# Performance work log

Hardware: AMD Instinct MI355X
Metric: run time of the kernel (lower is better)

The kernel has to match this reference:

```python
import jax, jax.numpy as jnp
import numpy as np
from jax import lax

ASPACE = 500
HEAD = 2
TEMP = 0.8
GEPS = 1e-20
LOG2PI = float(np.log(2.0 * np.pi))


def gru_cell(x, h, Wih, Whh, bih, bhh):
    # torch GRUCell math
    gi = x @ Wih.T + bih
    gh = h @ Whh.T + bhh
    i_r, i_z, i_n = jnp.split(gi, 3, axis=-1)
    h_r, h_z, h_n = jnp.split(gh, 3, axis=-1)
    r = jax.nn.sigmoid(i_r + h_r)
    z = jax.nn.sigmoid(i_z + h_z)
    n = jnp.tanh(i_n + r * h_n)
    return (1.0 - z) * n + z * h


def setup_inputs() -> dict:
    key = jax.random.key(0)
    ks = jax.random.split(key, 16)
    B, T, D, E = 128, 128, 300, 1024
    s = 0.05
    nrm = lambda k, shp: s * jax.random.normal(k, shp, dtype=jnp.float32)
    return {
        "x": jax.random.normal(ks[0], (B, T, D), dtype=jnp.float32),
        "lengths": jnp.full((B,), T, dtype=jnp.int32),  # full-length sequences
        "train": 1,
        # rl_rnn = GRUCell(300, 300)
        "Wih_cell": nrm(ks[1], (3 * D, D)),
        "Whh_cell": nrm(ks[2], (3 * D, D)),
        "bih_cell": nrm(ks[3], (3 * D,)),
        "bhh_cell": nrm(ks[4], (3 * D,)),
        # linear_rl_image_mus: 600 -> 1000
        "Wmu": nrm(ks[5], (ASPACE * HEAD, 2 * D)),
        "bmu": nrm(ks[6], (ASPACE * HEAD,)),
        # linear_logvars: 600 -> 2
        "Wlv": nrm(ks[7], (HEAD, 2 * D)),
        "blv": nrm(ks[8], (HEAD,)),
        # rnn = GRU(300, 1024, 1 layer)
        "Wih_rnn": nrm(ks[9], (3 * E, D)),
        "Whh_rnn": nrm(ks[10], (3 * E, E)),
        "bih_rnn": nrm(ks[11], (3 * E,)),
        "bhh_rnn": nrm(ks[12], (3 * E,)),
        # BatchNorm1d(1024)
        "bn_gamma": jnp.ones((E,), dtype=jnp.float32),
        "bn_beta": jnp.zeros((E,), dtype=jnp.float32),
    }


def _gumbel(key, shape):
    u = jax.random.uniform(key, shape, dtype=jnp.float32)
    return -jnp.log(-jnp.log(u + GEPS) + GEPS)


def reference(x, lengths, train, Wih_cell, Whh_cell, bih_cell, bhh_cell,
              Wmu, bmu, Wlv, blv, Wih_rnn, Whh_rnn, bih_rnn, bhh_rnn,
              bn_gamma, bn_beta):
    # train path only (train==1): stochastic gumbel-softmax + Normal sampling
    B, T, D = x.shape
    E = bn_gamma.shape[0]
    x = lax.stop_gradient(x)  # torch: x = x.detach()

    nk = jax.random.split(jax.random.key(42), 4)
    g_soft = _gumbel(nk[0], (T, B * HEAD, ASPACE))   # gumbel for softmax perturbation
    g_cat = _gumbel(nk[1], (T, B * HEAD, ASPACE))    # gumbel-max trick == multinomial
    eps1 = jax.random.normal(nk[2], (T, B, HEAD), dtype=jnp.float32)  # dist.sample()
    eps2 = jax.random.normal(nk[3], (T, B, HEAD), dtype=jnp.float32)  # second dist.sample() for log_prob

    arange_a = jnp.arange(ASPACE, dtype=jnp.float32)

    def step(hx, inputs):
        img, g, gc, e1, e2 = inputs  # img: [B,300]
        hx = gru_cell(img, hx, Wih_cell, Whh_cell, bih_cell, bhh_cell)
        cat = jax.nn.relu(jnp.concatenate([img, hx], axis=1))  # [B,600]
        mu = cat @ Wmu.T + bmu                                  # [B,1000]
        lv = jax.nn.softplus(cat @ Wlv.T + blv)                 # [B,2]
        logits = mu.reshape(B * HEAD, ASPACE)
        y = jax.nn.softmax((logits + g) / TEMP, axis=-1)
        ind = jnp.argmax(jnp.log(y) + gc, axis=-1)              # multinomial(y, 1)
        prob = jnp.take_along_axis(y, ind[:, None], axis=1)[:, 0]
        one_hot = jax.nn.one_hot(ind, ASPACE, dtype=y.dtype)
        y_hard = lax.stop_gradient(one_hot - y) + y             # straight-through
        action = (arange_a * y_hard).sum(-1).reshape(B, HEAD) / ASPACE  # [B,2]
        std = jnp.exp(0.5 * lv)                                 # [B,2]
        s1 = action + std * e1                                  # img_att sample
        s2 = action + std * e2                                  # sample used in log_prob
        logp = -0.5 * ((s2 - action) / std) ** 2 - jnp.log(std) - 0.5 * LOG2PI
        att = 20.0 * jax.nn.sigmoid(s1)                         # [B,2]
        text = (img.reshape(B, HEAD, D // HEAD) * att[:, :, None]).reshape(B, D)
        return hx, (action, jnp.log(prob).reshape(B, HEAD), logp, text)

    hx0 = jnp.zeros((B, D), dtype=x.dtype)
    xs = (x.transpose(1, 0, 2), g_soft, g_cat, eps1, eps2)
    _, (act, slog, logp, texts) = lax.scan(step, hx0, xs)
    # torch stacking/reshapes
    sampled_log_img_all = slog.transpose(1, 0, 2).reshape(B, HEAD, T)  # stack dim1 then view(B,H,T)
    action_imgs_all = act.transpose(1, 2, 0)                           # [B,2,T]
    log_all = logp.transpose(1, 2, 0)                                  # [B,2,T]

    # second-stage GRU over reconstructed sequence [T,B,300]
    def gru_step(h, xt):
        h = gru_cell(xt, h, Wih_rnn, Whh_rnn, bih_rnn, bhh_rnn)
        return h, h

    _, outs = lax.scan(gru_step, jnp.zeros((B, E), dtype=x.dtype), texts)  # [T,B,E]
    outs = outs.transpose(1, 0, 2)                                         # [B,T,E]
    last = outs[jnp.arange(B), lengths - 1]                                # gather last valid step

    # BatchNorm1d (training mode: batch stats, biased variance)
    mean = last.mean(axis=0)
    var = ((last - mean) ** 2).mean(axis=0)
    feature_end = bn_gamma * (last - mean) / jnp.sqrt(var + 1e-5) + bn_beta
    return (feature_end, sampled_log_img_all, action_imgs_all, log_all)
```

## Files before the change

### kernel.cpp

```cpp
#include <hip/hip_runtime.h>
#include <stdint.h>

#define TT 128
#define BB 128
#define DD 300
#define EE 1024
#define GG 900
#define NMU 1008
#define ASP 500
#define KP 608

#define OUT_SLOG 131072
#define OUT_ACT  163840
#define OUT_LOGP 196608

typedef unsigned int u32x4 __attribute__((ext_vector_type(4)));

__host__ __device__ static inline uint32_t rotl32(uint32_t x, int r){
  return (x << r) | (x >> (32 - r));
}

__host__ __device__ static inline void tf2x32(uint32_t k0, uint32_t k1,
                                              uint32_t x0, uint32_t x1,
                                              uint32_t* o0, uint32_t* o1){
  uint32_t ks2 = k0 ^ k1 ^ 0x1BD11BDAu;
#define TFR(r) { x0 += x1; x1 = rotl32(x1, r); x1 ^= x0; }
  x0 += k0; x1 += k1;
  TFR(13) TFR(15) TFR(26) TFR(6)
  x0 += k1; x1 += ks2 + 1u;
  TFR(17) TFR(29) TFR(16) TFR(24)
  x0 += ks2; x1 += k0 + 2u;
  TFR(13) TFR(15) TFR(26) TFR(6)
  x0 += k0; x1 += k1 + 3u;
  TFR(17) TFR(29) TFR(16) TFR(24)
  x0 += k1; x1 += ks2 + 4u;
  TFR(13) TFR(15) TFR(26) TFR(6)
  x0 += ks2; x1 += k0 + 5u;
#undef TFR
  *o0 = x0; *o1 = x1;
}

__device__ static inline uint32_t rng32(uint32_t k0, uint32_t k1, uint32_t idx){
  uint32_t a, b;
  tf2x32(k0, k1, 0u, idx, &a, &b);
  return a ^ b;
}

__device__ static inline float u01(uint32_t bits){
  return __uint_as_float((bits >> 9) | 0x3f800000u) - 1.0f;
}

__device__ static inline float jgumbel(uint32_t k0, uint32_t k1, uint32_t idx){
  float u = u01(rng32(k0, k1, idx));
  float l1 = logf(u + 1e-20f);
  return -logf(-l1 + 1e-20f);
}

__device__ static inline float erfinv32(float x){
  float w = -log1pf(-x * x);
  float p;
  if (w < 5.0f){
    w = w - 2.5f;
    p = 2.81022636e-08f;
    p = 3.43273939e-07f  + p * w;
    p = -3.5233877e-06f  + p * w;
    p = -4.39150654e-06f + p * w;
    p = 0.00021858087f   + p * w;
    p = -0.00125372503f  + p * w;
    p = -0.00417768164f  + p * w;
    p = 0.246640727f     + p * w;
    p = 1.50140941f      + p * w;
  } else {
    w = sqrtf(w) - 3.0f;
    p = -0.000200214257f;
    p = 0.000100950558f  + p * w;
    p = 0.00134934322f   + p * w;
    p = -0.00367342844f  + p * w;
    p = 0.00573950773f   + p * w;
    p = -0.0076224613f   + p * w;
    p = 0.00943887047f   + p * w;
    p = 1.00167406f      + p * w;
    p = 2.83297682f      + p * w;
  }
  return p * x;
}

__device__ static inline float jnormal(uint32_t k0, uint32_t k1, uint32_t idx){
  float u = u01(rng32(k0, k1, idx));
  const float lo = -0.99999994f;
  float v = u * 2.0f + lo;
  v = fmaxf(lo, v);
  return 1.41421356237f * erfinv32(v);
}

__device__ static inline float jsigmoid(float x){
  return 1.0f / (1.0f + expf(-x));
}

__device__ static inline unsigned short f2bf(float f){
  uint32_t u = __float_as_uint(f);
  uint32_t r = (u + 0x7fffu + ((u >> 16) & 1u)) >> 16;
  return (unsigned short)r;
}
__device__ static inline float bf2f(unsigned short h){
  return __uint_as_float((uint32_t)h << 16);
}

__device__ static inline u32x4 load_b128_llc(const void* p){
  u32x4 r;
  asm volatile("global_load_dwordx4 %0, %1, off sc0 sc1"
               : "=v"(r) : "v"(p) : "memory");
  return r;
}
__device__ static inline void store_b128_llc(void* p, u32x4 v){
  asm volatile("global_store_dwordx4 %0, %1, off sc0 sc1"
               :: "v"(p), "v"(v) : "memory");
}
__device__ static inline unsigned poll_u32_llc(const void* p){
  unsigned r;
  asm volatile("global_load_dword %0, %1, off sc0 sc1\n\ts_waitcnt vmcnt(0)"
               : "=v"(r) : "v"(p) : "memory");
  return r;
}
__device__ static inline void store_u32_llc(void* p, unsigned v){
  asm volatile("global_store_dword %0, %1, off sc0 sc1"
               :: "v"(p), "v"(v) : "memory");
}

#define WAITV(N) do{ asm volatile("s_waitcnt vmcnt(" #N ")" ::: "memory"); \
                     __builtin_amdgcn_sched_barrier(0); }while(0)

#define FMA4(ACC, S, B) { ACC.x += (S)*(B).x; ACC.y += (S)*(B).y; \
                          ACC.z += (S)*(B).z; ACC.w += (S)*(B).w; }

__global__ __launch_bounds__(256) void k_gemm_gi(
    const float* __restrict__ X, const float* __restrict__ W,
    const float* __restrict__ bias, float* __restrict__ C)
{
  __shared__ float As[16][132];
  __shared__ float Bs[16][68];
  const int tid = threadIdx.x;
  const int rbase = blockIdx.y * 128;
  const int cbase = blockIdx.x * 64;
  const int tx = tid & 15, ty = tid >> 4;
  const int sr = tid >> 2, sq = tid & 3;
  const int wj = cbase + sr;

  float4 acc[8];
#pragma unroll
  for (int i = 0; i < 8; ++i) acc[i] = (float4){0,0,0,0};

  for (int k0 = 0; k0 < 304; k0 += 16){
    const int k = k0 + sq * 4;
#pragma unroll
    for (int i = 0; i < 2; ++i){
      const int row = sr + i * 64;
      const int rg = rbase + row;
      float4 va = {0,0,0,0};
      if (k < DD) va = *(const float4*)(X + ((long)(rg & 127) * TT + (rg >> 7)) * DD + k);
      As[sq*4+0][row] = va.x; As[sq*4+1][row] = va.y;
      As[sq*4+2][row] = va.z; As[sq*4+3][row] = va.w;
    }
    {
      float4 vb = {0,0,0,0};
      if (k < DD && wj < GG) vb = *(const float4*)(W + (long)wj * DD + k);
      Bs[sq*4+0][sr] = vb.x; Bs[sq*4+1][sr] = vb.y;
      Bs[sq*4+2][sr] = vb.z; Bs[sq*4+3][sr] = vb.w;
    }
    __syncthreads();
#pragma unroll
    for (int kk = 0; kk < 16; ++kk){
      const float4 b  = *(const float4*)&Bs[kk][tx * 4];
      const float4 a0 = *(const float4*)&As[kk][ty * 8];
      const float4 a1 = *(const float4*)&As[kk][ty * 8 + 4];
      FMA4(acc[0], a0.x, b); FMA4(acc[1], a0.y, b);
      FMA4(acc[2], a0.z, b); FMA4(acc[3], a0.w, b);
      FMA4(acc[4], a1.x, b); FMA4(acc[5], a1.y, b);
      FMA4(acc[6], a1.z, b); FMA4(acc[7], a1.w, b);
    }
    __syncthreads();
  }
  const int ci = cbase + tx * 4;
  float bv[4];
#pragma unroll
  for (int j = 0; j < 4; ++j) bv[j] = (ci + j < GG) ? bias[ci + j] : 0.0f;
#pragma unroll
  for (int i = 0; i < 8; ++i){
    const int r = rbase + ty * 8 + i;
    float vals[4] = {acc[i].x + bv[0], acc[i].y + bv[1],
                     acc[i].z + bv[2], acc[i].w + bv[3]};
    float* crow = C + (long)r * GG;
    if (ci + 3 < GG){
      float4 st = {vals[0], vals[1], vals[2], vals[3]};
      *(float4*)(crow + ci) = st;
    } else {
#pragma unroll
      for (int j = 0; j < 4; ++j) if (ci + j < GG) crow[ci + j] = vals[j];
    }
  }
}

__global__ __launch_bounds__(256) void k_cvt_Amu(
    const float* __restrict__ X, const float* __restrict__ HX,
    unsigned short* __restrict__ Ah, unsigned short* __restrict__ Al)
{
  const long i = (long)blockIdx.x * 256 + threadIdx.x;
  const int r = (int)(i / 152), g = (int)(i - (long)r * 152);
  const int k = g * 4;
  const int b = r & 127, t = r >> 7;
  float4 v = {0,0,0,0};
  if (k < 300)      v = *(const float4*)(X + ((long)b * TT + t) * DD + k);
  else if (k < 600) v = *(const float4*)(HX + (long)r * DD + (k - 300));
  float vv[4] = {fmaxf(v.x,0.f), fmaxf(v.y,0.f), fmaxf(v.z,0.f), fmaxf(v.w,0.f)};
  unsigned short hi[4], lo[4];
#pragma unroll
  for (int j = 0; j < 4; ++j){
    hi[j] = f2bf(vv[j]);
    lo[j] = f2bf(vv[j] - bf2f(hi[j]));
  }
  const long off = (long)r * KP + k;
  *(uint2*)(Ah + off) = *(const uint2*)hi;
  *(uint2*)(Al + off) = *(const uint2*)lo;
}

__global__ __launch_bounds__(256) void k_cvt_Wmu(
    const float* __restrict__ Wmu, const float* __restrict__ Wlv,
    unsigned short* __restrict__ Wh, unsigned short* __restrict__ Wl)
{
  const long i = (long)blockIdx.x * 256 + threadIdx.x;
  const int r = (int)(i / 152), g = (int)(i - (long)r * 152);
  const int k = g * 4;
  float4 v = {0,0,0,0};
  if (k < 600){
    if (r < 1000)      v = *(const float4*)(Wmu + (long)r * 600 + k);
    else if (r < 1002) v = *(const float4*)(Wlv + (long)(r - 1000) * 600 + k);
  }
  float vv[4] = {v.x, v.y, v.z, v.w};
  unsigned short hi[4], lo[4];
#pragma unroll
  for (int j = 0; j < 4; ++j){
    hi[j] = f2bf(vv[j]);
    lo[j] = f2bf(vv[j] - bf2f(hi[j]));
  }
  const long off = (long)r * KP + k;
  *(uint2*)(Wh + off) = *(const uint2*)hi;
  *(uint2*)(Wl + off) = *(const uint2*)lo;
}

__global__ __launch_bounds__(256) void k_bias_mu(
    const float* __restrict__ bmu, const float* __restrict__ blv,
    float* __restrict__ bias)
{
  const int i = blockIdx.x * 256 + threadIdx.x;
  if (i < 1024){
    float v = 0.0f;
    if (i < 1000) v = bmu[i];
    else if (i < 1002) v = blv[i - 1000];
    bias[i] = v;
  }
}

__global__ __launch_bounds__(256) void k_gemm_mf(
    const unsigned short* __restrict__ Ah, const unsigned short* __restrict__ Al,
    const unsigned short* __restrict__ Bh, const unsigned short* __restrict__ Bl,
    const float* __restrict__ bias, float* __restrict__ C)
{
  __shared__ __align__(16) unsigned short sAh[128][40], sAl[128][40];
  __shared__ __align__(16) unsigned short sBh[64][40], sBl[64][40];
  const int tid = threadIdx.x;
  const int cbase = blockIdx.x * 64, rbase = blockIdx.y * 128;
  const int wave = tid >> 6, wm = wave >> 1, wn = wave & 1;
  const int lane = tid & 63, lo = lane & 15, hi4 = lane >> 4;

  using frag = __attribute__((ext_vector_type(8))) short;
  using f32x4 = __attribute__((ext_vector_type(4))) float;
  f32x4 acc[4][2];
#pragma unroll
  for (int a = 0; a < 4; ++a)
#pragma unroll
    for (int c = 0; c < 2; ++c) acc[a][c] = (f32x4){0.f,0.f,0.f,0.f};

  const int arow = tid >> 1, akh = (tid & 1) * 16;
  const int brow = tid >> 2, bkh = (tid & 3) * 8;

  for (int kb = 0; kb < 19; ++kb){
    const int k0 = kb * 32;
    __syncthreads();
    {
      const unsigned short* pa = Ah + (long)(rbase + arow) * KP + k0 + akh;
      *(uint4*)&sAh[arow][akh]     = *(const uint4*)pa;
      *(uint4*)&sAh[arow][akh + 8] = *(const uint4*)(pa + 8);
      const unsigned short* pl = Al + (long)(rbase + arow) * KP + k0 + akh;
      *(uint4*)&sAl[arow][akh]     = *(const uint4*)pl;
      *(uint4*)&sAl[arow][akh + 8] = *(const uint4*)(pl + 8);
      *(uint4*)&sBh[brow][bkh] = *(const uint4*)(Bh + (long)(cbase + brow) * KP + k0 + bkh);
      *(uint4*)&sBl[brow][bkh] = *(const uint4*)(Bl + (long)(cbase + brow) * KP + k0 + bkh);
    }
    __syncthreads();
    frag bh0 = *(const frag*)&sBh[wn*32 + lo][hi4*8];
    frag bh1 = *(const frag*)&sBh[wn*32 + 16 + lo][hi4*8];
    frag bl0 = *(const frag*)&sBl[wn*32 + lo][hi4*8];
    frag bl1 = *(const frag*)&sBl[wn*32 + 16 + lo][hi4*8];
#pragma unroll
    for (int fr = 0; fr < 4; ++fr){
      frag ah = *(const frag*)&sAh[wm*64 + fr*16 + lo][hi4*8];
      frag al = *(const frag*)&sAl[wm*64 + fr*16 + lo][hi4*8];
      acc[fr][0] = __builtin_amdgcn_mfma_f32_16x16x32_bf16(ah, bh0, acc[fr][0], 0, 0, 0);
      acc[fr][0] = __builtin_amdgcn_mfma_f32_16x16x32_bf16(al, bh0, acc[fr][0], 0, 0, 0);
      acc[fr][0] = __builtin_amdgcn_mfma_f32_16x16x32_bf16(ah, bl0, acc[fr][0], 0, 0, 0);
      acc[fr][0] = __builtin_amdgcn_mfma_f32_16x16x32_bf16(al, bl0, acc[fr][0], 0, 0, 0);
      acc[fr][1] = __builtin_amdgcn_mfma_f32_16x16x32_bf16(ah, bh1, acc[fr][1], 0, 0, 0);
      acc[fr][1] = __builtin_amdgcn_mfma_f32_16x16x32_bf16(al, bh1, acc[fr][1], 0, 0, 0);
      acc[fr][1] = __builtin_amdgcn_mfma_f32_16x16x32_bf16(ah, bl1, acc[fr][1], 0, 0, 0);
      acc[fr][1] = __builtin_amdgcn_mfma_f32_16x16x32_bf16(al, bl1, acc[fr][1], 0, 0, 0);
    }
  }
#pragma unroll
  for (int fr = 0; fr < 4; ++fr)
#pragma unroll
    for (int fc = 0; fc < 2; ++fc){
      const int col = cbase + wn*32 + fc*16 + lo;
      if (col < NMU){
        const float bv = bias[col];
        const int r0 = rbase + wm*64 + fr*16 + hi4*4;
#pragma unroll
        for (int j = 0; j < 4; ++j)
          C[(long)(r0 + j) * NMU + col] = acc[fr][fc][j] + bv;
      }
    }
}

__global__ __launch_bounds__(256) void k_pack_w3(
    const float* __restrict__ W, unsigned short* __restrict__ Wb3)
{
  const int g = blockIdx.x * 256 + threadIdx.x;
  if (g >= 245760) return;
  const int k4 = g % 80;
  const int r2 = g / 80;
  const int row = r2 % 64;
  const int r3 = r2 / 64;
  const int s = r3 % 3;
  const int js = r3 / 3;
  const int wid = (js < 15) ? 19 : 15;
  const int jj0 = js * 19;
  unsigned short o4[4];
#pragma unroll
  for (int e = 0; e < 4; ++e){
    const int k = k4 * 4 + e;
    float v = 0.0f;
    if (row < 3 * wid && k < 300){
      const int gate = row / wid, col = row - gate * wid;
      v = W[(long)(gate * 300 + jj0 + col) * 300 + k];
    }
    const unsigned short w1 = f2bf(v);
    const float r1 = v - bf2f(w1);
    const unsigned short w2 = f2bf(r1);
    const float r2f = r1 - bf2f(w2);
    const unsigned short w3 = f2bf(r2f);
    o4[e] = (s == 0) ? w1 : ((s == 1) ? w2 : w3);
  }
  *(uint2*)(Wb3 + ((long)(js * 3 + s) * 64 + row) * 320 + k4 * 4) = *(const uint2*)o4;
}

#define S1PAD 304

__global__ __launch_bounds__(256, 1) void k_stage1(
    const unsigned short* __restrict__ Wb3, const float* __restrict__ bhh,
    const float* __restrict__ gi_all, float* __restrict__ hx_all,
    float* __restrict__ hex, unsigned int* __restrict__ flagsA)
{
  __shared__ __align__(16) float hs[8][S1PAD];
  __shared__ __align__(16) unsigned short hb[3][8][320];
  __shared__ float ghs[512];
  const int tid = threadIdx.x;
  const int bid = blockIdx.x;
  const int bq = bid >> 4, js = bid & 15;
  const int b0 = bq * 8;
  const int wid = (js < 15) ? 19 : 15;
  const int jj0 = js * 19;
  const int NC = 3 * wid;

  const int wave = tid >> 6, lane = tid & 63;
  const int lo = lane & 15, hi = lane >> 4;

  using frag = __attribute__((ext_vector_type(8))) short;
  using f32x4v = __attribute__((ext_vector_type(4))) float;

  frag wfr[3][10];
  {
    const int row = wave * 16 + lo;
#pragma unroll
    for (int s = 0; s < 3; ++s)
#pragma unroll
      for (int kf = 0; kf < 10; ++kf)
        wfr[s][kf] = *(const frag*)(Wb3 + ((long)(js * 3 + s) * 64 + row) * 320
                                         + kf * 32 + hi * 8);
  }

  const bool gact = tid < 8 * wid;
  const int grow = gact ? (tid / wid) : 0;
  const int gcol = gact ? (tid - grow * wid) : 0;
  const int gjj = jj0 + gcol;
  float bhr = 0.f, bhz = 0.f, bhn = 0.f;
  if (gact){ bhr = bhh[gjj]; bhz = bhh[DD + gjj]; bhn = bhh[2*DD + gjj]; }

  for (int i = tid; i < 8 * S1PAD; i += 256) ((float*)hs)[i] = 0.f;
  for (int i = tid; i < 3840; i += 256) ((unsigned int*)hb)[i] = 0u;
  __syncthreads();

  unsigned int* myflag = flagsA + bid * 16;

  for (int t = 0; t < TT; ++t){
    float gir = 0.f, giz = 0.f, gin = 0.f;
    if (gact){
      const float* gp = gi_all + ((long)t * BB + b0 + grow) * GG;
      gir = gp[gjj]; giz = gp[DD + gjj]; gin = gp[2*DD + gjj];
    }

    f32x4v a0 = {0,0,0,0}, a1 = {0,0,0,0}, a2 = {0,0,0,0};
#pragma unroll
    for (int kf = 0; kf < 10; ++kf){
      frag h1 = *(const frag*)&hb[0][lo & 7][kf * 32 + hi * 8];
      frag h2 = *(const frag*)&hb[1][lo & 7][kf * 32 + hi * 8];
      frag h3 = *(const frag*)&hb[2][lo & 7][kf * 32 + hi * 8];
      a0 = __builtin_amdgcn_mfma_f32_16x16x32_bf16(h1, wfr[0][kf], a0, 0, 0, 0);
      a1 = __builtin_amdgcn_mfma_f32_16x16x32_bf16(h1, wfr[1][kf], a1, 0, 0, 0);
      a2 = __builtin_amdgcn_mfma_f32_16x16x32_bf16(h1, wfr[2][kf], a2, 0, 0, 0);
      a0 = __builtin_amdgcn_mfma_f32_16x16x32_bf16(h2, wfr[0][kf], a0, 0, 0, 0);
      a1 = __builtin_amdgcn_mfma_f32_16x16x32_bf16(h2, wfr[1][kf], a1, 0, 0, 0);
      a2 = __builtin_amdgcn_mfma_f32_16x16x32_bf16(h2, wfr[2][kf], a2, 0, 0, 0);
      a0 = __builtin_amdgcn_mfma_f32_16x16x32_bf16(h3, wfr[0][kf], a0, 0, 0, 0);
      a1 = __builtin_amdgcn_mfma_f32_16x16x32_bf16(h3, wfr[1][kf], a1, 0, 0, 0);
      a2 = __builtin_amdgcn_mfma_f32_16x16x32_bf16(h3, wfr[2][kf], a2, 0, 0, 0);
    }
    {
      const int nc = wave * 16 + lo;
      if (hi < 2 && nc < NC){
#pragma unroll
        for (int j = 0; j < 4; ++j)
          ghs[nc * 8 + hi * 4 + j] = (a0[j] + a1[j]) + a2[j];
      }
    }
    __syncthreads();

    const int par = t & 1;
    if (gact){
      const float r = jsigmoid(gir + ghs[(0 * wid + gcol) * 8 + grow] + bhr);
      const float z = jsigmoid(giz + ghs[(1 * wid + gcol) * 8 + grow] + bhz);
      const float n = tanhf(gin + r * (ghs[(2 * wid + gcol) * 8 + grow] + bhn));
      const float hn = (1.0f - z) * n + z * hs[grow][gjj];
      hx_all[((long)t * BB + b0 + grow) * DD + gjj] = hn;
      if (t < TT - 1)
        store_u32_llc(hex + ((long)par * BB + b0 + grow) * S1PAD + gjj,
                      __float_as_uint(hn));
    }

    if (t < TT - 1){
      asm volatile("s_waitcnt vmcnt(0)" ::: "memory");
      __syncthreads();
      if (tid == 0) store_u32_llc(myflag, (unsigned)(t + 1));
      if (tid < 16){
        const unsigned int* fp = flagsA + (bq * 16 + tid) * 16;
        unsigned v = poll_u32_llc(fp);
        while (v < (unsigned)(t + 1)){
          __builtin_amdgcn_s_sleep(1);
          v = poll_u32_llc(fp);
        }
      }
      __syncthreads();
      {
        const float* src = hex + (long)par * BB * S1PAD + (long)b0 * S1PAD;
        const int gA = tid, gB = tid + 256, gC = tid + 512;
        const int rA = gA / 76, cA = gA - rA * 76;
        const int rB = gB / 76, cB = gB - rB * 76;
        int rC = 0, cC = 0;
        u32x4 vA = load_b128_llc(src + (long)rA * S1PAD + cA * 4);
        u32x4 vB = load_b128_llc(src + (long)rB * S1PAD + cB * 4);
        u32x4 vC = (u32x4){0,0,0,0};
        if (gC < 608){
          rC = gC / 76; cC = gC - rC * 76;
          vC = load_b128_llc(src + (long)rC * S1PAD + cC * 4);
        }
        WAITV(0);
#define CONV_STORE(rr, cc, vv) do{ \
        float f0 = __uint_as_float(vv[0]), f1 = __uint_as_float(vv[1]); \
        float f2v = __uint_as_float(vv[2]), f3 = __uint_as_float(vv[3]); \
        if ((cc) == 75){ f0 = 0.f; f1 = 0.f; f2v = 0.f; f3 = 0.f; } \
        *(u32x4*)&hs[rr][(cc) * 4] = vv; \
        float fv[4] = {f0, f1, f2v, f3}; \
        unsigned short s1[4], s2[4], s3[4]; \
        _Pragma("unroll") \
        for (int j = 0; j < 4; ++j){ \
          s1[j] = f2bf(fv[j]); \
          const float r1 = fv[j] - bf2f(s1[j]); \
          s2[j] = f2bf(r1); \
          s3[j] = f2bf(r1 - bf2f(s2[j])); \
        } \
        *(uint2*)&hb[0][rr][(cc) * 4] = *(const uint2*)s1; \
        *(uint2*)&hb[1][rr][(cc) * 4] = *(const uint2*)s2; \
        *(uint2*)&hb[2][rr][(cc) * 4] = *(const uint2*)s3; \
      }while(0)
        CONV_STORE(rA, cA, vA);
        CONV_STORE(rB, cB, vB);
        if (gC < 608) CONV_STORE(rC, cC, vC);
#undef CONV_STORE
      }
      __syncthreads();
    }
  }
}

__global__ __launch_bounds__(256) void k_sample(
    const float* __restrict__ X, const float* __restrict__ mu_all,
    unsigned short* __restrict__ tF, float* __restrict__ out,
    const uint32_t k0a, const uint32_t k0b, const uint32_t k1a, const uint32_t k1b,
    const uint32_t k2a, const uint32_t k2b, const uint32_t k3a, const uint32_t k3b)
{
  const int r = blockIdx.x;
  const int t = r >> 7, b = r & 127;
  const int tid = threadIdx.x;
  const int h = tid >> 7, lane = tid & 127;
  const int wv = tid >> 6;
  __shared__ float redw[4];
  __shared__ int   redi4[4];
  __shared__ float yw[2], lyw[2], att_s[2];

  const uint32_t rowbase = (uint32_t)((t * 256 + b * 2 + h) * 500);
  float zv[4], ev[4];
  float lmax = -3.0e38f;
#pragma unroll
  for (int s = 0; s < 4; ++s){
    const int a = lane + s * 128;
    float z = -3.0e38f;
    if (a < ASP){
      float g = jgumbel(k0a, k0b, rowbase + (uint32_t)a);
      float m = mu_all[(long)r * NMU + h * ASP + a];
      z = (m + g) / 0.8f;
    }
    zv[s] = z;
    lmax = fmaxf(lmax, z);
  }
  {
    float wm = lmax;
#pragma unroll
    for (int o = 32; o > 0; o >>= 1) wm = fmaxf(wm, __shfl_xor(wm, o));
    if ((tid & 63) == 0) redw[wv] = wm;
  }
  __syncthreads();
  const float mx = fmaxf(redw[h * 2], redw[h * 2 + 1]);
  __syncthreads();

  float lsum = 0.0f;
#pragma unroll
  for (int s = 0; s < 4; ++s){
    const int a = lane + s * 128;
    float e = 0.0f;
    if (a < ASP) e = expf(zv[s] - mx);
    ev[s] = e;
    lsum += e;
  }
  {
    float wsum = lsum;
#pragma unroll
    for (int o = 32; o > 0; o >>= 1) wsum += __shfl_xor(wsum, o);
    if ((tid & 63) == 0) redw[wv] = wsum;
  }
  __syncthreads();
  const float S = redw[h * 2] + redw[h * 2 + 1];
  __syncthreads();

  float bestv = -3.0e38f;
  int besti = 0x7fffffff;
#pragma unroll
  for (int s = 0; s < 4; ++s){
    const int a = lane + s * 128;
    if (a < ASP){
      float y = ev[s] / S;
      float ly = logf(y);
      float gc = jgumbel(k1a, k1b, rowbase + (uint32_t)a);
      float val = ly + gc;
      if (val > bestv){ bestv = val; besti = a; }
    }
  }
  {
    float bv = bestv; int bi = besti;
#pragma unroll
    for (int o = 32; o > 0; o >>= 1){
      float v2 = __shfl_xor(bv, o);
      int   i2 = __shfl_xor(bi, o);
      if (v2 > bv || (v2 == bv && i2 < bi)){ bv = v2; bi = i2; }
    }
    if ((tid & 63) == 0){ redw[wv] = bv; redi4[wv] = bi; }
  }
  __syncthreads();
  int ind;
  {
    const float v0 = redw[h * 2], v1 = redw[h * 2 + 1];
    const int   i0 = redi4[h * 2], i1 = redi4[h * 2 + 1];
    ind = (v1 > v0 || (v1 == v0 && i1 < i0)) ? i1 : i0;
  }
#pragma unroll
  for (int s = 0; s < 4; ++s){
    const int a = lane + s * 128;
    if (a == ind){
      float y = ev[s] / S;
      yw[h] = y;
      lyw[h] = logf(y);
    }
  }
  __syncthreads();
  if (lane == 0){
    const float yv = yw[h];
    const float ly = lyw[h];
    const float yh = (1.0f - yv) + yv;
    const float act = ((float)ind * yh) / 500.0f;
    const float lvr = mu_all[(long)r * NMU + 1000 + h];
    const float lv = fmaxf(lvr, 0.0f) + log1pf(expf(-fabsf(lvr)));
    const float sd = expf(0.5f * lv);
    const uint32_t ei = (uint32_t)(r * 2 + h);
    const float e1 = jnormal(k2a, k2b, ei);
    const float e2 = jnormal(k3a, k3b, ei);
    const float s1 = act + sd * e1;
    const float s2 = act + sd * e2;
    const float dd = (s2 - act) / sd;
    const float lp = -0.5f * (dd * dd) - logf(sd) - 0.9189385332046727f;
    const float attv = 20.0f * jsigmoid(s1);
    out[OUT_SLOG + (long)b * 256 + t * 2 + h]  = ly;
    out[OUT_ACT  + (long)b * 256 + h * 128 + t] = act;
    out[OUT_LOGP + (long)b * 256 + h * 128 + t] = lp;
    att_s[h] = attv;
  }
  __syncthreads();
  const float* xr = X + ((long)b * TT + t) * DD;
  if (tid < 40){
    unsigned short pk[8];
#pragma unroll
    for (int e = 0; e < 8; ++e){
      const int idx = tid * 8 + e;
      float v = 0.0f;
      if (idx < 300) v = xr[idx] * att_s[idx / 150];
      pk[e] = f2bf(v);
    }
    unsigned short* dst = tF + (((long)t * 8 + (b >> 4)) * 40 + tid) * 128
                             + (b & 15) * 8;
    *(uint4*)dst = *(const uint4*)pk;
  }
}

__global__ __launch_bounds__(256) void k_cvt_whh(
    const float* __restrict__ W, unsigned short* __restrict__ O)
{
  const int i = blockIdx.x * 256 + threadIdx.x;
  O[i] = f2bf(W[i]);
}

__global__ __launch_bounds__(256) void k_cvt_wih(
    const float* __restrict__ W, unsigned short* __restrict__ O)
{
  const int i = blockIdx.x * 256 + threadIdx.x;
  const int rw = i / 320, c = i - rw * 320;
  O[i] = (c < DD) ? f2bf(W[(long)rw * DD + c]) : (unsigned short)0;
}

#define NBLK2 128
#define WPITCH 2704

__global__ __launch_bounds__(512) void k_stage2(
    const unsigned short* __restrict__ tF,
    const unsigned short* __restrict__ Whb,
    const unsigned short* __restrict__ Wib,
    const float* __restrict__ bih, const float* __restrict__ bhh,
    const int* __restrict__ lengths,
    unsigned short* __restrict__ hF0, unsigned short* __restrict__ hF1,
    float* __restrict__ last,
    unsigned int* __restrict__ flags)
{
  __shared__ __align__(16) char lds[152320];
  unsigned short* Wl = (unsigned short*)lds;
  char* Al = lds + 129792;
  unsigned short* Tl = (unsigned short*)(lds + 150272);

  const int tid = threadIdx.x;
  const int bid = blockIdx.x;
  const int m = bid >> 6, n = bid & 63;
  const int e0 = n * 16, mrow = m * 64;
  const int wave = tid >> 6, wg = wave >> 2, wvr = wave & 3;
  const int lane = tid & 63, lo = lane & 15, hi = lane >> 4;
  const int tidg = tid & 255;

  for (int s = tid; s < 48 * 168; s += 512){
    const int row = s / 168, q = s - row * 168;
    const int g = row >> 4, nn = row & 15;
    const long wrow = (long)g * EE + e0 + nn;
    uint4 v;
    if (q < 128) v = *(const uint4*)(Whb + wrow * EE + q * 8);
    else         v = *(const uint4*)(Wib + wrow * 320 + (q - 128) * 8);
    *(uint4*)((char*)Wl + (long)row * WPITCH + q * 16) = v;
  }

  const int e = e0 + lo;
  const float bR = bih[e] + bhh[e];
  const float bZ = bih[EE + e] + bhh[EE + e];
  const float biN = bih[2*EE + e];
  const float bhN = bhh[2*EE + e];
  int li[4]; float hp[4];
#pragma unroll
  for (int j = 0; j < 4; ++j){
    const int brow = wvr * 16 + hi * 4 + j;
    int l = lengths[mrow + brow] - 1; if (l < 0) l += TT;
    li[j] = l; hp[j] = 0.0f;
  }
  __syncthreads();

  using frag = __attribute__((ext_vector_type(8))) short;
  using f32x4 = __attribute__((ext_vector_type(4))) float;

  const int rg = m * 4 + wvr;
  int boff[3];
#pragma unroll
  for (int g = 0; g < 3; ++g) boff[g] = (g * 16 + lo) * WPITCH + hi * 16;

  const long tBase = ((long)rg * 40 + (wg ? 24 : 0) + hi) * 128 + lo * 8;
  const long hBase = (long)rg * 16384 + (long)(wg * 64 + hi) * 128 + lo * 8;

  unsigned int* flagp = flags + (m << 6) + n;

  for (int t = 0; t < TT; ++t){
    const unsigned short* hFin = (t & 1) ? hF1 : hF0;
    unsigned short* hFout = (t & 1) ? hF0 : hF1;
    const unsigned short* tA = tF + (long)t * 8 * 40 * 128 + tBase;
    const unsigned short* hA = hFin + hBase;

    f32x4 aR = {0,0,0,0}, aZ = {0,0,0,0}, aNH = {0,0,0,0}, aNI = {0,0,0,0};

    auto chunkD = [&](int cc, u32x4 a0v, u32x4 a1v, bool hid){
      frag a0 = *(frag*)&a0v;
      frag a1 = *(frag*)&a1v;
      const char* wb = (const char*)Wl + cc * 128;
      frag b00 = *(const frag*)(wb + boff[0]);
      frag b10 = *(const frag*)(wb + boff[1]);
      frag b20 = *(const frag*)(wb + boff[2]);
      frag b01 = *(const frag*)(wb + boff[0] + 64);
      frag b11 = *(const frag*)(wb + boff[1] + 64);
      frag b21 = *(const frag*)(wb + boff[2] + 64);
      aR = __builtin_amdgcn_mfma_f32_16x16x32_bf16(a0, b00, aR, 0, 0, 0);
      aZ = __builtin_amdgcn_mfma_f32_16x16x32_bf16(a0, b10, aZ, 0, 0, 0);
      if (hid) aNH = __builtin_amdgcn_mfma_f32_16x16x32_bf16(a0, b20, aNH, 0, 0, 0);
      else     aNI = __builtin_amdgcn_mfma_f32_16x16x32_bf16(a0, b20, aNI, 0, 0, 0);
      aR = __builtin_amdgcn_mfma_f32_16x16x32_bf16(a1, b01, aR, 0, 0, 0);
      aZ = __builtin_amdgcn_mfma_f32_16x16x32_bf16(a1, b11, aZ, 0, 0, 0);
      if (hid) aNH = __builtin_amdgcn_mfma_f32_16x16x32_bf16(a1, b21, aNH, 0, 0, 0);
      else     aNI = __builtin_amdgcn_mfma_f32_16x16x32_bf16(a1, b21, aNI, 0, 0, 0);
    };

    {
      u32x4 t0a = load_b128_llc(tA);
      u32x4 t0b = load_b128_llc(tA + 512);
      u32x4 t1a = load_b128_llc(tA + 1024);
      u32x4 t1b = load_b128_llc(tA + 1536);
      if (wg == 0){
        u32x4 t2a = load_b128_llc(tA + 2048);
        u32x4 t2b = load_b128_llc(tA + 2560);
        WAITV(4); chunkD(16, t0a, t0b, false);
        WAITV(2); chunkD(17, t1a, t1b, false);
        WAITV(0); chunkD(18, t2a, t2b, false);
      } else {
        WAITV(2); chunkD(19, t0a, t0b, false);
        WAITV(0); chunkD(20, t1a, t1b, false);
      }
    }

    if (t > 0){
      if (tid < 16){
        const unsigned int* fp = flags + (m << 6) + tid * 4;
        for (;;){
          u32x4 f = load_b128_llc(fp);
          WAITV(0);
          if (f[0] >= (unsigned)t && f[1] >= (unsigned)t &&
              f[2] >= (unsigned)t && f[3] >= (unsigned)t) break;
          __builtin_amdgcn_s_sleep(2);
        }
      }
      __syncthreads();

      u32x4 h0a = load_b128_llc(hA +    0), h0b = load_b128_llc(hA +  512);
      u32x4 h1a = load_b128_llc(hA + 1024), h1b = load_b128_llc(hA + 1536);
      u32x4 h2a = load_b128_llc(hA + 2048), h2b_ = load_b128_llc(hA + 2560);
      u32x4 h3a = load_b128_llc(hA + 3072), h3b = load_b128_llc(hA + 3584);
      u32x4 h4a = load_b128_llc(hA + 4096), h4b = load_b128_llc(hA + 4608);
      u32x4 h5a = load_b128_llc(hA + 5120), h5b = load_b128_llc(hA + 5632);
      u32x4 h6a = load_b128_llc(hA + 6144), h6b = load_b128_llc(hA + 6656);
      u32x4 h7a = load_b128_llc(hA + 7168), h7b = load_b128_llc(hA + 7680);
      const int cb = wg * 8;
      WAITV(14); chunkD(cb + 0, h0a, h0b, true);
      WAITV(12); chunkD(cb + 1, h1a, h1b, true);
      WAITV(10); chunkD(cb + 2, h2a, h2b_, true);
      WAITV(8);  chunkD(cb + 3, h3a, h3b, true);
      WAITV(6);  chunkD(cb + 4, h4a, h4b, true);
      WAITV(4);  chunkD(cb + 5, h5a, h5b, true);
      WAITV(2);  chunkD(cb + 6, h6a, h6b, true);
      WAITV(0);  chunkD(cb + 7, h7a, h7b, true);
    }

    __syncthreads();
    if (wg == 1){
      char* dst = Al + tidg * 80;
      *(f32x4*)(dst)      = aR;
      *(f32x4*)(dst + 16) = aZ;
      *(f32x4*)(dst + 32) = aNH;
      *(f32x4*)(dst + 48) = aNI;
    }
    __syncthreads();
    if (wg == 0){
      const char* src = Al + tidg * 80;
      const f32x4 pR  = *(const f32x4*)(src);
      const f32x4 pZ  = *(const f32x4*)(src + 16);
      const f32x4 pNH = *(const f32x4*)(src + 32);
      const f32x4 pNI = *(const f32x4*)(src + 48);
#pragma unroll
      for (int j = 0; j < 4; ++j){
        aR[j] += pR[j]; aZ[j] += pZ[j]; aNH[j] += pNH[j]; aNI[j] += pNI[j];
      }
#pragma unroll
      for (int j = 0; j < 4; ++j){
        const int brow = wvr * 16 + hi * 4 + j;
        const float r = jsigmoid(aR[j] + bR);
        const float z = jsigmoid(aZ[j] + bZ);
        const float nn2 = tanhf(aNI[j] + biN + r * (aNH[j] + bhN));
        const float hn = (1.0f - z) * nn2 + z * hp[j];
        hp[j] = hn;
        Tl[brow * 16 + lo] = f2bf(hn);
        if (t == li[j]) last[(long)(mrow + brow) * EE + e] = hn;
      }
    }

    if (t < TT - 1){
      __syncthreads();
      if (tid < 128){
        const int rgp = tid >> 5;
        const int kbp = (tid >> 4) & 1;
        const int lop = tid & 15;
        u32x4 v = *(const u32x4*)(Tl + (rgp * 16 + lop) * 16 + kbp * 8);
        store_b128_llc(hFout + ((long)(m * 4 + rgp) * 128 + (n * 2 + kbp)) * 128
                             + lop * 8, v);
      }
      asm volatile("s_waitcnt vmcnt(0)" ::: "memory");
      __syncthreads();
      if (tid == 0) store_u32_llc(flagp, (unsigned)(t + 1));
    }
  }
}

__global__ __launch_bounds__(256) void k_bn_stats(
    const float* __restrict__ last, float* __restrict__ mv)
{
  const int e = blockIdx.x * 256 + threadIdx.x;
  if (e >= EE) return;
  float s = 0.0f;
  for (int b = 0; b < BB; ++b) s += last[(long)b * EE + e];
  const float mean = s / 128.0f;
  float v = 0.0f;
  for (int b = 0; b < BB; ++b){ float d = last[(long)b * EE + e] - mean; v += d * d; }
  mv[e] = mean;
  mv[EE + e] = v / 128.0f;
}

__global__ __launch_bounds__(256) void k_bn_apply(
    const float* __restrict__ last, const float* __restrict__ mv,
    const float* __restrict__ gamma, const float* __restrict__ beta,
    float* __restrict__ out)
{
  const int gid = blockIdx.x * 256 + threadIdx.x;
  const int e = gid & 1023;
  const float xm = last[gid] - mv[e];
  out[gid] = gamma[e] * xm / sqrtf(mv[EE + e] + 1e-5f) + beta[e];
}

extern "C" void kernel_launch(void* const* d_in, const int* in_sizes, int n_in,
                              void* d_out, int out_size, void* d_ws, size_t ws_size,
                              hipStream_t stream)
{
  (void)in_sizes; (void)n_in; (void)out_size;
  const float* x     = (const float*)d_in[0];
  const int*   lens  = (const int*)d_in[1];
  const float* Wih_c = (const float*)d_in[3];
  const float* Whh_c = (const float*)d_in[4];
  const float* bih_c = (const float*)d_in[5];
  const float* bhh_c = (const float*)d_in[6];
  const float* Wmu   = (const float*)d_in[7];
  const float* bmu   = (const float*)d_in[8];
  const float* Wlv   = (const float*)d_in[9];
  const float* blv   = (const float*)d_in[10];
  const float* Wih_r = (const float*)d_in[11];
  const float* Whh_r = (const float*)d_in[12];
  const float* bih_r = (const float*)d_in[13];
  const float* bhh_r = (const float*)d_in[14];
  const float* gam   = (const float*)d_in[15];
  const float* bet   = (const float*)d_in[16];
  float* out = (float*)d_out;

  uint32_t nk[4][2];
  for (uint32_t i = 0; i < 4; ++i) tf2x32(0u, 42u, 0u, i, &nk[i][0], &nk[i][1]);

  float* ws = (float*)d_ws;
  size_t off = 0;
  float* U       = ws + off; off += 16515072;
  float* hx_all  = ws + off; off += 4915200;
  float* lastb   = ws + off; off += 131072;
  float* mv      = ws + off; off += 2048;
  float* hex     = ws + off; off += 77824;
  float* biasM   = ws + off; off += 1024;
  unsigned int* flags  = (unsigned int*)(ws + off); off += 2048;
  unsigned int* flagsA = (unsigned int*)(ws + off); off += 4096;
  unsigned short* tF  = (unsigned short*)(ws + off); off += 2621440;
  unsigned short* hF0 = (unsigned short*)(ws + off); off += 65536;
  unsigned short* hF1 = (unsigned short*)(ws + off); off += 65536;
  unsigned short* Whb = (unsigned short*)(ws + off); off += 1572864;
  unsigned short* Wib = (unsigned short*)(ws + off); off += 491520;
  unsigned short* Wb3 = (unsigned short*)(ws + off); off += 491520;
  unsigned short* WmH = (unsigned short*)(ws + off); off += 311296;
  unsigned short* WmL = (unsigned short*)(ws + off); off += 311296;
  unsigned short* AmH = (unsigned short*)(ws + off); off += 4980736;
  unsigned short* AmL = (unsigned short*)(ws + off); off += 4980736;
  if (ws_size < off * sizeof(float)) return;

  hipMemsetAsync(flags, 0, 2048 * sizeof(unsigned int), stream);
  hipMemsetAsync(flagsA, 0, 4096 * sizeof(unsigned int), stream);

  k_cvt_whh<<<dim3(12288), 256, 0, stream>>>(Whh_r, Whb);
  k_cvt_wih<<<dim3(3840), 256, 0, stream>>>(Wih_r, Wib);
  k_pack_w3<<<dim3(960), 256, 0, stream>>>(Whh_c, Wb3);
  k_cvt_Wmu<<<dim3(608), 256, 0, stream>>>(Wmu, Wlv, WmH, WmL);
  k_bias_mu<<<dim3(4), 256, 0, stream>>>(bmu, blv, biasM);

  k_gemm_gi<<<dim3(15, 128), 256, 0, stream>>>(x, Wih_c, bih_c, U);
  k_stage1<<<dim3(256), 256, 0, stream>>>(Wb3, bhh_c, U, hx_all, hex, flagsA);

  k_cvt_Amu<<<dim3(9728), 256, 0, stream>>>(x, hx_all, AmH, AmL);
  k_gemm_mf<<<dim3(16, 128), 256, 0, stream>>>(AmH, AmL, WmH, WmL, biasM, U);
  k_sample<<<dim3(16384), 256, 0, stream>>>(x, U, tF, out,
      nk[0][0], nk[0][1], nk[1][0], nk[1][1],
      nk[2][0], nk[2][1], nk[3][0], nk[3][1]);

  k_stage2<<<dim3(NBLK2), 512, 0, stream>>>(tF, Whb, Wib, bih_r, bhh_r, lens,
                                            hF0, hF1, lastb, flags);

  k_bn_stats<<<dim3(4), 256, 0, stream>>>(lastb, mv);
  k_bn_apply<<<dim3(512), 256, 0, stream>>>(lastb, mv, gam, bet, out);
}
```

Baseline: 1.493 ms.

## Keep recurrent GRU weights in registers and split K across four wave groups

The stage-2 GRU kernel now loads each wave's slice of the hidden-to-hidden bf16 weights into registers once, instead of reading them from LDS every timestep. Only the input weights stay in LDS, which shrinks the LDS footprint. Work is repartitioned so each wave covers two 16-row batch tiles over a quarter of the K dimension. Three waves then write partial sums to LDS for a single wave group to reduce before applying the gate nonlinearities. The aim is to remove per-step LDS weight traffic and raise MFMA reuse of the B fragments. The cost is much higher register pressure and a larger LDS reduction step.

```diff
diff --git a/kernel.cpp b/kernel.cpp
--- a/kernel.cpp
+++ b/kernel.cpp
@@ -663,7 +663,8 @@
 }
 
 #define NBLK2 128
-#define WPITCH 2704
+#define PBASE 31488
+#define TLBASE 80640
 
 __global__ __launch_bounds__(512) void k_stage2(
     const unsigned short* __restrict__ tF,
@@ -675,99 +676,128 @@
     float* __restrict__ last,
     unsigned int* __restrict__ flags)
 {
-  __shared__ __align__(16) char lds[152320];
-  unsigned short* Wl = (unsigned short*)lds;
-  char* Al = lds + 129792;
-  unsigned short* Tl = (unsigned short*)(lds + 150272);
+  __shared__ __align__(16) char lds[82688];
+  unsigned short* WlT = (unsigned short*)lds;
+  char* Pb = lds + PBASE;
+  unsigned short* Tl = (unsigned short*)(lds + TLBASE);
 
   const int tid = threadIdx.x;
   const int bid = blockIdx.x;
   const int m = bid >> 6, n = bid & 63;
   const int e0 = n * 16, mrow = m * 64;
-  const int wave = tid >> 6, wg = wave >> 2, wvr = wave & 3;
+  const int wave = tid >> 6, mt = wave >> 2, kg = wave & 3;
   const int lane = tid & 63, lo = lane & 15, hi = lane >> 4;
-  const int tidg = tid & 255;
-
-  for (int s = tid; s < 48 * 168; s += 512){
-    const int row = s / 168, q = s - row * 168;
+
+  using frag = __attribute__((ext_vector_type(8))) short;
+  using f32x4 = __attribute__((ext_vector_type(4))) float;
+
+  for (int s = tid; s < 48 * 40; s += 512){
+    const int row = s / 40, q = s - row * 40;
     const int g = row >> 4, nn = row & 15;
-    const long wrow = (long)g * EE + e0 + nn;
-    uint4 v;
-    if (q < 128) v = *(const uint4*)(Whb + wrow * EE + q * 8);
-    else         v = *(const uint4*)(Wib + wrow * 320 + (q - 128) * 8);
-    *(uint4*)((char*)Wl + (long)row * WPITCH + q * 16) = v;
-  }
+    *(uint4*)((char*)WlT + row * 656 + q * 16) =
+        *(const uint4*)(Wib + (long)(g * EE + e0 + nn) * 320 + q * 8);
+  }
+
+  frag wfrH[4][3][2];
+#pragma unroll
+  for (int i = 0; i < 4; ++i)
+#pragma unroll
+    for (int g = 0; g < 3; ++g)
+#pragma unroll
+      for (int kf = 0; kf < 2; ++kf)
+        wfrH[i][g][kf] = *(const frag*)(Whb + ((long)g * EE + e0 + lo) * EE
+                                        + (kg * 4 + i) * 64 + kf * 32 + hi * 8);
 
   const int e = e0 + lo;
   const float bR = bih[e] + bhh[e];
   const float bZ = bih[EE + e] + bhh[EE + e];
   const float biN = bih[2*EE + e];
   const float bhN = bhh[2*EE + e];
-  int li[4]; float hp[4];
-#pragma unroll
-  for (int j = 0; j < 4; ++j){
-    const int brow = wvr * 16 + hi * 4 + j;
-    int l = lengths[mrow + brow] - 1; if (l < 0) l += TT;
-    li[j] = l; hp[j] = 0.0f;
-  }
+  int li[2][4]; float hp[2][4];
+#pragma unroll
+  for (int sub = 0; sub < 2; ++sub)
+#pragma unroll
+    for (int j = 0; j < 4; ++j){
+      const int brow = (mt * 2 + sub) * 16 + hi * 4 + j;
+      int l = lengths[mrow + brow] - 1; if (l < 0) l += TT;
+      li[sub][j] = l; hp[sub][j] = 0.0f;
+    }
   __syncthreads();
 
-  using frag = __attribute__((ext_vector_type(8))) short;
-  using f32x4 = __attribute__((ext_vector_type(4))) float;
-
-  const int rg = m * 4 + wvr;
-  int boff[3];
-#pragma unroll
-  for (int g = 0; g < 3; ++g) boff[g] = (g * 16 + lo) * WPITCH + hi * 16;
-
-  const long tBase = ((long)rg * 40 + (wg ? 24 : 0) + hi) * 128 + lo * 8;
-  const long hBase = (long)rg * 16384 + (long)(wg * 64 + hi) * 128 + lo * 8;
+  const int rg0 = m * 4 + mt * 2, rg1 = rg0 + 1;
+  const long hOff0 = (long)rg0 * 16384 + hi * 128 + lo * 8;
+  const long hOff1 = (long)rg1 * 16384 + hi * 128 + lo * 8;
+  const long tOff0 = (long)rg0 * 5120 + hi * 128 + lo * 8;
+  const long tOff1 = (long)rg1 * 5120 + hi * 128 + lo * 8;
 
   unsigned int* flagp = flags + (m << 6) + n;
+
+#define TEXB(g, kf, cp) (*(const frag*)((char*)WlT + ((g)*16 + lo)*656 \
+                          + ((cp)*64 + (kf)*32 + hi*8)*2))
 
   for (int t = 0; t < TT; ++t){
     const unsigned short* hFin = (t & 1) ? hF1 : hF0;
     unsigned short* hFout = (t & 1) ? hF0 : hF1;
-    const unsigned short* tA = tF + (long)t * 8 * 40 * 128 + tBase;
-    const unsigned short* hA = hFin + hBase;
-
-    f32x4 aR = {0,0,0,0}, aZ = {0,0,0,0}, aNH = {0,0,0,0}, aNI = {0,0,0,0};
-
-    auto chunkD = [&](int cc, u32x4 a0v, u32x4 a1v, bool hid){
-      frag a0 = *(frag*)&a0v;
-      frag a1 = *(frag*)&a1v;
-      const char* wb = (const char*)Wl + cc * 128;
-      frag b00 = *(const frag*)(wb + boff[0]);
-      frag b10 = *(const frag*)(wb + boff[1]);
-      frag b20 = *(const frag*)(wb + boff[2]);
-      frag b01 = *(const frag*)(wb + boff[0] + 64);
-      frag b11 = *(const frag*)(wb + boff[1] + 64);
-      frag b21 = *(const frag*)(wb + boff[2] + 64);
-      aR = __builtin_amdgcn_mfma_f32_16x16x32_bf16(a0, b00, aR, 0, 0, 0);
-      aZ = __builtin_amdgcn_mfma_f32_16x16x32_bf16(a0, b10, aZ, 0, 0, 0);
-      if (hid) aNH = __builtin_amdgcn_mfma_f32_16x16x32_bf16(a0, b20, aNH, 0, 0, 0);
-      else     aNI = __builtin_amdgcn_mfma_f32_16x16x32_bf16(a0, b20, aNI, 0, 0, 0);
-      aR = __builtin_amdgcn_mfma_f32_16x16x32_bf16(a1, b01, aR, 0, 0, 0);
-      aZ = __builtin_amdgcn_mfma_f32_16x16x32_bf16(a1, b11, aZ, 0, 0, 0);
-      if (hid) aNH = __builtin_amdgcn_mfma_f32_16x16x32_bf16(a1, b21, aNH, 0, 0, 0);
-      else     aNI = __builtin_amdgcn_mfma_f32_16x16x32_bf16(a1, b21, aNI, 0, 0, 0);
+    const unsigned short* tB = tF + (long)t * 5120 * 8;
+
+    f32x4 accR[2], accZ[2], accNH[2], accNI[2];
+#pragma unroll
+    for (int s = 0; s < 2; ++s){
+      accR[s] = (f32x4){0,0,0,0}; accZ[s] = (f32x4){0,0,0,0};
+      accNH[s] = (f32x4){0,0,0,0}; accNI[s] = (f32x4){0,0,0,0};
+    }
+
+    auto mfm6 = [&](frag a0k0, frag a0k1, frag a1k0, frag a1k1,
+                    frag b00, frag b01, frag b10, frag b11,
+                    frag b20, frag b21, bool hid){
+      accR[0] = __builtin_amdgcn_mfma_f32_16x16x32_bf16(a0k0, b00, accR[0], 0, 0, 0);
+      accR[0] = __builtin_amdgcn_mfma_f32_16x16x32_bf16(a0k1, b01, accR[0], 0, 0, 0);
+      accR[1] = __builtin_amdgcn_mfma_f32_16x16x32_bf16(a1k0, b00, accR[1], 0, 0, 0);
+      accR[1] = __builtin_amdgcn_mfma_f32_16x16x32_bf16(a1k1, b01, accR[1], 0, 0, 0);
+      accZ[0] = __builtin_amdgcn_mfma_f32_16x16x32_bf16(a0k0, b10, accZ[0], 0, 0, 0);
+      accZ[0] = __builtin_amdgcn_mfma_f32_16x16x32_bf16(a0k1, b11, accZ[0], 0, 0, 0);
+      accZ[1] = __builtin_amdgcn_mfma_f32_16x16x32_bf16(a1k0, b10, accZ[1], 0, 0, 0);
+      accZ[1] = __builtin_amdgcn_mfma_f32_16x16x32_bf16(a1k1, b11, accZ[1], 0, 0, 0);
+      if (hid){
+        accNH[0] = __builtin_amdgcn_mfma_f32_16x16x32_bf16(a0k0, b20, accNH[0], 0, 0, 0);
+        accNH[0] = __builtin_amdgcn_mfma_f32_16x16x32_bf16(a0k1, b21, accNH[0], 0, 0, 0);
+        accNH[1] = __builtin_amdgcn_mfma_f32_16x16x32_bf16(a1k0, b20, accNH[1], 0, 0, 0);
+        accNH[1] = __builtin_amdgcn_mfma_f32_16x16x32_bf16(a1k1, b21, accNH[1], 0, 0, 0);
+      } else {
+        accNI[0] = __builtin_amdgcn_mfma_f32_16x16x32_bf16(a0k0, b20, accNI[0], 0, 0, 0);
+        accNI[0] = __builtin_amdgcn_mfma_f32_16x16x32_bf16(a0k1, b21, accNI[0], 0, 0, 0);
+        accNI[1] = __builtin_amdgcn_mfma_f32_16x16x32_bf16(a1k0, b20, accNI[1], 0, 0, 0);
+        accNI[1] = __builtin_amdgcn_mfma_f32_16x16x32_bf16(a1k1, b21, accNI[1], 0, 0, 0);
+      }
     };
 
-    {
-      u32x4 t0a = load_b128_llc(tA);
-      u32x4 t0b = load_b128_llc(tA + 512);
-      u32x4 t1a = load_b128_llc(tA + 1024);
-      u32x4 t1b = load_b128_llc(tA + 1536);
-      if (wg == 0){
-        u32x4 t2a = load_b128_llc(tA + 2048);
-        u32x4 t2b = load_b128_llc(tA + 2560);
-        WAITV(4); chunkD(16, t0a, t0b, false);
-        WAITV(2); chunkD(17, t1a, t1b, false);
-        WAITV(0); chunkD(18, t2a, t2b, false);
-      } else {
-        WAITV(2); chunkD(19, t0a, t0b, false);
-        WAITV(0); chunkD(20, t1a, t1b, false);
-      }
+    if (kg == 0){
+      u32x4 a00 = load_b128_llc(tB + tOff0);
+      u32x4 a01 = load_b128_llc(tB + tOff0 + 512);
+      u32x4 a10 = load_b128_llc(tB + tOff1);
+      u32x4 a11 = load_b128_llc(tB + tOff1 + 512);
+      u32x4 b00 = load_b128_llc(tB + tOff0 + 1024);
+      u32x4 b01 = load_b128_llc(tB + tOff0 + 1536);
+      u32x4 b10 = load_b128_llc(tB + tOff1 + 1024);
+      u32x4 b11 = load_b128_llc(tB + tOff1 + 1536);
+      WAITV(4);
+      mfm6(*(frag*)&a00, *(frag*)&a01, *(frag*)&a10, *(frag*)&a11,
+           TEXB(0,0,0), TEXB(0,1,0), TEXB(1,0,0), TEXB(1,1,0),
+           TEXB(2,0,0), TEXB(2,1,0), false);
+      WAITV(0);
+      mfm6(*(frag*)&b00, *(frag*)&b01, *(frag*)&b10, *(frag*)&b11,
+           TEXB(0,0,1), TEXB(0,1,1), TEXB(1,0,1), TEXB(1,1,1),
+           TEXB(2,0,1), TEXB(2,1,1), false);
+    } else {
+      const int cp = kg + 1;
+      u32x4 a00 = load_b128_llc(tB + tOff0 + cp * 1024);
+      u32x4 a01 = load_b128_llc(tB + tOff0 + cp * 1024 + 512);
+      u32x4 a10 = load_b128_llc(tB + tOff1 + cp * 1024);
+      u32x4 a11 = load_b128_llc(tB + tOff1 + cp * 1024 + 512);
+      WAITV(0);
+      mfm6(*(frag*)&a00, *(frag*)&a01, *(frag*)&a10, *(frag*)&a11,
+           TEXB(0,0,cp), TEXB(0,1,cp), TEXB(1,0,cp), TEXB(1,1,cp),
+           TEXB(2,0,cp), TEXB(2,1,cp), false);
     }
 
     if (t > 0){
@@ -783,55 +813,78 @@
       }
       __syncthreads();
 
-      u32x4 h0a = load_b128_llc(hA +    0), h0b = load_b128_llc(hA +  512);
-      u32x4 h1a = load_b128_llc(hA + 1024), h1b = load_b128_llc(hA + 1536);
-      u32x4 h2a = load_b128_llc(hA + 2048), h2b_ = load_b128_llc(hA + 2560);
-      u32x4 h3a = load_b128_llc(hA + 3072), h3b = load_b128_llc(hA + 3584);
-      u32x4 h4a = load_b128_llc(hA + 4096), h4b = load_b128_llc(hA + 4608);
-      u32x4 h5a = load_b128_llc(hA + 5120), h5b = load_b128_llc(hA + 5632);
-      u32x4 h6a = load_b128_llc(hA + 6144), h6b = load_b128_llc(hA + 6656);
-      u32x4 h7a = load_b128_llc(hA + 7168), h7b = load_b128_llc(hA + 7680);
-      const int cb = wg * 8;
-      WAITV(14); chunkD(cb + 0, h0a, h0b, true);
-      WAITV(12); chunkD(cb + 1, h1a, h1b, true);
-      WAITV(10); chunkD(cb + 2, h2a, h2b_, true);
-      WAITV(8);  chunkD(cb + 3, h3a, h3b, true);
-      WAITV(6);  chunkD(cb + 4, h4a, h4b, true);
-      WAITV(4);  chunkD(cb + 5, h5a, h5b, true);
-      WAITV(2);  chunkD(cb + 6, h6a, h6b, true);
-      WAITV(0);  chunkD(cb + 7, h7a, h7b, true);
-    }
-
+      u32x4 ha[4][2][2];
+#pragma unroll
+      for (int i = 0; i < 4; ++i){
+        const long co = (long)(kg * 4 + i) * 1024;
+        ha[i][0][0] = load_b128_llc(hFin + hOff0 + co);
+        ha[i][0][1] = load_b128_llc(hFin + hOff0 + co + 512);
+        ha[i][1][0] = load_b128_llc(hFin + hOff1 + co);
+        ha[i][1][1] = load_b128_llc(hFin + hOff1 + co + 512);
+      }
+      WAITV(12);
+      mfm6(*(frag*)&ha[0][0][0], *(frag*)&ha[0][0][1],
+           *(frag*)&ha[0][1][0], *(frag*)&ha[0][1][1],
+           wfrH[0][0][0], wfrH[0][0][1], wfrH[0][1][0], wfrH[0][1][1],
+           wfrH[0][2][0], wfrH[0][2][1], true);
+      WAITV(8);
+      mfm6(*(frag*)&ha[1][0][0], *(frag*)&ha[1][0][1],
+           *(frag*)&ha[1][1][0], *(frag*)&ha[1][1][1],
+           wfrH[1][0][0], wfrH[1][0][1], wfrH[1][1][0], wfrH[1][1][1],
+           wfrH[1][2][0], wfrH[1][2][1], true);
+      WAITV(4);
+      mfm6(*(frag*)&ha[2][0][0], *(frag*)&ha[2][0][1],
+           *(frag*)&ha[2][1][0], *(frag*)&ha[2][1][1],
+           wfrH[2][0][0], wfrH[2][0][1], wfrH[2][1][0], wfrH[2][1][1],
+           wfrH[2][2][0], wfrH[2][2][1], true);
+      WAITV(0);
+      mfm6(*(frag*)&ha[3][0][0], *(frag*)&ha[3][0][1],
+           *(frag*)&ha[3][1][0], *(frag*)&ha[3][1][1],
+           wfrH[3][0][0], wfrH[3][0][1], wfrH[3][1][0], wfrH[3][1][1],
+           wfrH[3][2][0], wfrH[3][2][1], true);
+    }
+
+    if (kg != 0){
+      char* dst = Pb + ((kg - 1) * 2 + mt) * 8192;
+#pragma unroll
+      for (int sub = 0; sub < 2; ++sub){
+        *(f32x4*)(dst + ((sub * 4 + 0) * 64 + lane) * 16) = accR[sub];
+        *(f32x4*)(dst + ((sub * 4 + 1) * 64 + lane) * 16) = accZ[sub];
+        *(f32x4*)(dst + ((sub * 4 + 2) * 64 + lane) * 16) = accNH[sub];
+        *(f32x4*)(dst + ((sub * 4 + 3) * 64 + lane) * 16) = accNI[sub];
+      }
+    }
     __syncthreads();
-    if (wg == 1){
-      char* dst = Al + tidg * 80;
-      *(f32x4*)(dst)      = aR;
-      *(f32x4*)(dst + 16) = aZ;
-      *(f32x4*)(dst + 32) = aNH;
-      *(f32x4*)(dst + 48) = aNI;
-    }
-    __syncthreads();
-    if (wg == 0){
-      const char* src = Al + tidg * 80;
-      const f32x4 pR  = *(const f32x4*)(src);
-      const f32x4 pZ  = *(const f32x4*)(src + 16);
-      const f32x4 pNH = *(const f32x4*)(src + 32);
-      const f32x4 pNI = *(const f32x4*)(src + 48);
-#pragma unroll
-      for (int j = 0; j < 4; ++j){
-        aR[j] += pR[j]; aZ[j] += pZ[j]; aNH[j] += pNH[j]; aNI[j] += pNI[j];
+    if (kg == 0){
+#pragma unroll
+      for (int p = 0; p < 3; ++p){
+        const char* src = Pb + (p * 2 + mt) * 8192;
+#pragma unroll
+        for (int sub = 0; sub < 2; ++sub){
+          const f32x4 pR  = *(const f32x4*)(src + ((sub*4 + 0) * 64 + lane) * 16);
+          const f32x4 pZ  = *(const f32x4*)(src + ((sub*4 + 1) * 64 + lane) * 16);
+          const f32x4 pNH = *(const f32x4*)(src + ((sub*4 + 2) * 64 + lane) * 16);
+          const f32x4 pNI = *(const f32x4*)(src + ((sub*4 + 3) * 64 + lane) * 16);
+#pragma unroll
+          for (int j = 0; j < 4; ++j){
+            accR[sub][j] += pR[j]; accZ[sub][j] += pZ[j];
+            accNH[sub][j] += pNH[j]; accNI[sub][j] += pNI[j];
+          }
+        }
       }
 #pragma unroll
-      for (int j = 0; j < 4; ++j){
-        const int brow = wvr * 16 + hi * 4 + j;
-        const float r = jsigmoid(aR[j] + bR);
-        const float z = jsigmoid(aZ[j] + bZ);
-        const float nn2 = tanhf(aNI[j] + biN + r * (aNH[j] + bhN));
-        const float hn = (1.0f - z) * nn2 + z * hp[j];
-        hp[j] = hn;
-        Tl[brow * 16 + lo] = f2bf(hn);
-        if (t == li[j]) last[(long)(mrow + brow) * EE + e] = hn;
-      }
+      for (int sub = 0; sub < 2; ++sub)
+#pragma unroll
+        for (int j = 0; j < 4; ++j){
+          const int brow = (mt * 2 + sub) * 16 + hi * 4 + j;
+          const float r = jsigmoid(accR[sub][j] + bR);
+          const float z = jsigmoid(accZ[sub][j] + bZ);
+          const float nn2 = tanhf(accNI[sub][j] + biN + r * (accNH[sub][j] + bhN));
+          const float hn = (1.0f - z) * nn2 + z * hp[sub][j];
+          hp[sub][j] = hn;
+          Tl[brow * 16 + lo] = f2bf(hn);
+          if (t == li[sub][j]) last[(long)(mrow + brow) * EE + e] = hn;
+        }
     }
 
     if (t < TT - 1){
@@ -849,6 +902,7 @@
       if (tid == 0) store_u32_llc(flagp, (unsigned)(t + 1));
     }
   }
+#undef TEXB
 }
 
 __global__ __launch_bounds__(256) void k_bn_stats(
```

Result: slower. 1.998 ms (+33.8%).
